# Performance work log

Hardware: AMD Instinct MI355X
Metric: run time of the kernel (lower is better)

## Reference

```python
import jax, jax.numpy as jnp
import numpy as np

B, S, D = 4, 4096, 128

def setup_inputs() -> dict:
    key = jax.random.key(0)
    kq, kk, kv = jax.random.split(key, 3)
    q = jax.random.normal(kq, (B, S, D), dtype=jnp.float32)
    k = jax.random.normal(kk, (B, S, D), dtype=jnp.float32)
    v = jax.random.normal(kv, (B, S, D), dtype=jnp.float32)
    return {"q": q, "k": k, "v": v}

def reference(q, k, v):
    d_model = q.shape[-1]
    scale = 1.0 / jnp.sqrt(jnp.asarray(d_model, q.dtype))
    # [B, S, S] scores
    scores = jnp.einsum('bqd,bkd->bqk', q, k) * scale
    s = q.shape[1]
    causal = jnp.tril(jnp.ones((s, s), dtype=bool))
    neg_inf = jnp.asarray(-jnp.inf, scores.dtype)
    scores = jnp.where(causal[None, :, :], scores, neg_inf)
    attn = jax.nn.softmax(scores, axis=-1)
    return jnp.einsum('bqk,bkd->bqd', attn, v)
```

## Files before the change

kernel.cpp:

```cpp
#include <hip/hip_runtime.h>


#define B_   4
#define S_   4096
#define D_   128
#define NT_  64
#define QT_  32
#define JB   128
#define W_   1056
#define SLOTS_PB 160
#define BLOB_SHORTS 16384
#define MASKVAL (-1.0e30f)

typedef __attribute__((ext_vector_type(8))) short bf16x8;
typedef __attribute__((ext_vector_type(4))) float f32x4;
typedef __attribute__((ext_vector_type(16))) float f32x16;

__device__ __forceinline__ short f2bf(float x) {
    unsigned u = __builtin_bit_cast(unsigned, x);
    unsigned r = (u + 0x7fffu + ((u >> 16) & 1u)) >> 16;
    return (short)r;
}
__device__ __forceinline__ float ex2(float x) { return __builtin_amdgcn_exp2f(x); }
__device__ __forceinline__ unsigned pkbf(float lo, float hi) {
    return (unsigned)(unsigned short)f2bf(lo) | ((unsigned)(unsigned short)f2bf(hi) << 16);
}
__device__ __forceinline__ float bf2f(short s) {
    return __builtin_bit_cast(float, ((unsigned)(unsigned short)s) << 16);
}
__device__ __forceinline__ void gl_lds16(const short* g, short* l) {
    __builtin_amdgcn_global_load_lds(
        (const __attribute__((address_space(1))) unsigned int*)g,
        (__attribute__((address_space(3))) unsigned int*)l, 16, 0, 0);
}
__device__ __forceinline__ int chunk_of(int v) { return (4 * v + 3) / 33; }

__global__ __launch_bounds__(256) void prep(const float* __restrict__ Qg,
                                            const float* __restrict__ Kg,
                                            const float* __restrict__ Vg,
                                            short* __restrict__ Qbf,
                                            short* __restrict__ KV)
{
    __shared__ short vt[64][40];
    const int id  = blockIdx.x;
    const int tid = threadIdx.x;
    const float SC = 0.12751740f;

    if (id < 1024) {
        const int b = id & 3, tile = (id >> 2) & 63, q4 = id >> 8;
        const int n = q4 * 16 + (tid >> 4);
        const int G = tid & 15;
        const size_t rowoff = ((size_t)b * S_ + (size_t)tile * 64 + n) * D_ + G * 8;
        short* blob = KV + (size_t)(b * NT_ + tile) * BLOB_SHORTS;
        {
            float4 a = *reinterpret_cast<const float4*>(Qg + rowoff);
            float4 c = *reinterpret_cast<const float4*>(Qg + rowoff + 4);
            bf16x8 v;
            v[0] = f2bf(a.x * SC); v[1] = f2bf(a.y * SC); v[2] = f2bf(a.z * SC); v[3] = f2bf(a.w * SC);
            v[4] = f2bf(c.x * SC); v[5] = f2bf(c.y * SC); v[6] = f2bf(c.z * SC); v[7] = f2bf(c.w * SC);
            *reinterpret_cast<bf16x8*>(Qbf + rowoff) = v;
        }
        {
            float4 a = *reinterpret_cast<const float4*>(Kg + rowoff);
            float4 c = *reinterpret_cast<const float4*>(Kg + rowoff + 4);
            bf16x8 v;
            v[0] = f2bf(a.x); v[1] = f2bf(a.y); v[2] = f2bf(a.z); v[3] = f2bf(a.w);
            v[4] = f2bf(c.x); v[5] = f2bf(c.y); v[6] = f2bf(c.z); v[7] = f2bf(c.w);
            const int p = (G & 8) | ((G & 7) ^ (n & 7));
            *reinterpret_cast<bf16x8*>(blob + n * 128 + p * 8) = v;
        }
    } else {
        const int u = id - 1024;
        const int b = u & 3, tile = (u >> 2) & 63, dq = u >> 8;
        short* blob = KV + (size_t)(b * NT_ + tile) * BLOB_SHORTS;
        {
            const int n = tid >> 2, c8 = tid & 3;
            const size_t off = ((size_t)b * S_ + (size_t)tile * 64 + n) * D_ + dq * 32 + c8 * 8;
            float4 a = *reinterpret_cast<const float4*>(Vg + off);
            float4 c = *reinterpret_cast<const float4*>(Vg + off + 4);
            bf16x8 v;
            v[0] = f2bf(a.x); v[1] = f2bf(a.y); v[2] = f2bf(a.z); v[3] = f2bf(a.w);
            v[4] = f2bf(c.x); v[5] = f2bf(c.y); v[6] = f2bf(c.z); v[7] = f2bf(c.w);
            *reinterpret_cast<bf16x8*>(&vt[n][c8 * 8]) = v;
        }
        __syncthreads();
        {
            const int dl = tid >> 3, G = tid & 7;
            const int d  = dq * 32 + dl;
            bf16x8 g;
#pragma unroll
            for (int i = 0; i < 8; ++i) g[i] = vt[G * 8 + i][dl];
            const int p = G ^ (d & 7);
            *reinterpret_cast<bf16x8*>(blob + 8192 + d * 64 + p * 8) = g;
        }
    }
}

__global__ __launch_bounds__(256, 2) void fa_bal(const short* __restrict__ Qbf,
                                                 const short* __restrict__ KV,
                                                 short* __restrict__ Opb,
                                                 float* __restrict__ Ml)
{
    __shared__ short lkv[2][BLOB_SHORTS];

    const int tid  = threadIdx.x;
    const int wv   = tid >> 6;
    const int lane = tid & 63;
    const int col  = lane & 31;
    const int half = lane >> 5;
    const int c7   = col & 7;

    const int batch = blockIdx.x & 3;
    const int j     = blockIdx.x >> 2;
    const int v0    = (33 * j) >> 2;
    const int v1    = (33 * (j + 1)) >> 2;

    int t = (int)((sqrtf((float)(4 * v0 + 1)) - 1.0f) * 0.5f);
    while ((t + 1) * (t + 2) <= v0) ++t;
    while (t * (t + 1) > v0) --t;
    int ktl = v0 - t * (t + 1);

    int base = 0;
    for (int tt = 0; tt < t; ++tt) {
        int a = chunk_of(tt * (tt + 1));
        int b2 = chunk_of((tt + 1) * (tt + 2) - 1);
        base += b2 - a + 1;
    }
    int slot = batch * SLOTS_PB + base + (j - chunk_of(t * (t + 1)));

    const size_t tilebase = (size_t)batch * NT_ * BLOB_SHORTS;
#define STAGE(KT, BUF) do {                                                   \
        const short* g_ = KV + tilebase + (size_t)(KT) * BLOB_SHORTS + tid * 8;\
        short* l_ = (BUF) + tid * 8;                                          \
        _Pragma("unroll")                                                     \
        for (int c_ = 0; c_ < 8; ++c_)                                        \
            gl_lds16(g_ + c_ * 2048, l_ + c_ * 2048);                         \
    } while (0)
#define LOADQ(T) do {                                                         \
        const short* qp_ = Qbf + ((size_t)batch * S_ + (size_t)(T) * 128      \
                                  + wv * 32 + col) * D_ + half * 8;           \
        _Pragma("unroll")                                                     \
        for (int c_ = 0; c_ < 8; ++c_)                                        \
            qf[c_] = *reinterpret_cast<const bf16x8*>(qp_ + c_ * 16);         \
    } while (0)

    bf16x8 qf[8];
    LOADQ(t);

    f32x16 acc[4];
#pragma unroll
    for (int i = 0; i < 4; ++i)
#pragma unroll
        for (int r = 0; r < 16; ++r) acc[i][r] = 0.f;
    float mrun = MASKVAL, lrun = 0.f;

    STAGE(ktl, lkv[0]);

    for (int v = v0; v < v1; ++v) {
        const short* cur = lkv[(v - v0) & 1];
        short* nxt = lkv[(v - v0 + 1) & 1];

        int nt = t, nktl = ktl + 1;
        if (nktl == 2 * t + 2) { nt = t + 1; nktl = 0; }

        __syncthreads();
        if (v + 1 < v1) STAGE(nktl, nxt);

        const short* lk = cur;
        const short* lv = cur + 8192;

        f32x16 st[2];
#pragma unroll
        for (int i = 0; i < 2; ++i)
#pragma unroll
            for (int r = 0; r < 16; ++r) st[i][r] = 0.f;
#pragma unroll
        for (int c = 0; c < 8; ++c) {
            const int G = 2 * c + half;
            const int p = (G & 8) | ((G & 7) ^ c7);
#pragma unroll
            for (int kt32 = 0; kt32 < 2; ++kt32) {
                const int n = kt32 * 32 + col;
                bf16x8 kf = *reinterpret_cast<const bf16x8*>(lk + n * 128 + p * 8);
                st[kt32] = __builtin_amdgcn_mfma_f32_32x32x16_bf16(kf, qf[c], st[kt32], 0, 0, 0);
            }
        }

        if (ktl >= 2 * t) {
            const int kbase = (ktl - 2 * t) * 64;
            const int qloc  = wv * 32 + col;
#pragma unroll
            for (int kt32 = 0; kt32 < 2; ++kt32)
#pragma unroll
                for (int r = 0; r < 16; ++r) {
                    const int kl = kt32 * 32 + (r & 3) + 8 * (r >> 2) + 4 * half;
                    if (kbase + kl > qloc) st[kt32][r] = MASKVAL;
                }
        }

        float mx = MASKVAL;
#pragma unroll
        for (int i = 0; i < 2; ++i)
#pragma unroll
            for (int r = 0; r < 16; ++r) mx = fmaxf(mx, st[i][r]);
        mx = fmaxf(mx, __shfl_xor(mx, 32));
        const float mnew = fmaxf(mrun, mx);
        const float al   = ex2(mrun - mnew);
        mrun = mnew;
        float sum = 0.f;
#pragma unroll
        for (int i = 0; i < 2; ++i)
#pragma unroll
            for (int r = 0; r < 16; ++r) {
                float pv = ex2(st[i][r] - mnew);
                st[i][r] = pv;
                sum += pv;
            }
        sum += __shfl_xor(sum, 32);
        lrun = lrun * al + sum;
#pragma unroll
        for (int i = 0; i < 4; ++i)
#pragma unroll
            for (int r = 0; r < 16; ++r) acc[i][r] *= al;

#pragma unroll
        for (int kt32 = 0; kt32 < 2; ++kt32) {
            unsigned pw[4][2];
#pragma unroll
            for (int w = 0; w < 4; ++w) {
                pw[w][0] = pkbf(st[kt32][4 * w],     st[kt32][4 * w + 1]);
                pw[w][1] = pkbf(st[kt32][4 * w + 2], st[kt32][4 * w + 3]);
            }
#pragma unroll
            for (int s1 = 0; s1 < 2; ++s1) {
                unsigned snd0 = pw[2 * s1 + 1 - half][0];
                unsigned snd1 = pw[2 * s1 + 1 - half][1];
                unsigned rcv0 = __shfl_xor((int)snd0, 32);
                unsigned rcv1 = __shfl_xor((int)snd1, 32);
                unsigned own0 = pw[2 * s1 + half][0];
                unsigned own1 = pw[2 * s1 + half][1];
                int4 wi;
                wi.x = (int)(half ? rcv0 : own0);
                wi.y = (int)(half ? rcv1 : own1);
                wi.z = (int)(half ? own0 : rcv0);
                wi.w = (int)(half ? own1 : rcv1);
                bf16x8 pf = __builtin_bit_cast(bf16x8, wi);
                const int G = 2 * (kt32 * 2 + s1) + half;
                const int p = G ^ c7;
#pragma unroll
                for (int dt = 0; dt < 4; ++dt) {
                    const int d = dt * 32 + col;
                    bf16x8 vf = *reinterpret_cast<const bf16x8*>(lv + d * 64 + p * 8);
                    acc[dt] = __builtin_amdgcn_mfma_f32_32x32x16_bf16(vf, pf, acc[dt], 0, 0, 0);
                }
            }
        }

        if (nktl == 0 || v + 1 == v1) {
            short* ob = Opb + (size_t)slot * (128 * D_) + tid * 64;
#pragma unroll
            for (int dt = 0; dt < 4; ++dt)
#pragma unroll
                for (int g = 0; g < 4; ++g) {
                    int2 w;
                    w.x = (int)pkbf(acc[dt][4 * g],     acc[dt][4 * g + 1]);
                    w.y = (int)pkbf(acc[dt][4 * g + 2], acc[dt][4 * g + 3]);
                    *reinterpret_cast<int2*>(ob + (dt * 4 + g) * 4) = w;
                }
            if (half == 0) {
                float* mlb = Ml + (size_t)slot * (128 * 2) + (wv * 32 + col) * 2;
                mlb[0] = mrun;
                mlb[1] = lrun;
            }
            if (v + 1 < v1) {
                int a = chunk_of(t * (t + 1));
                int b2 = chunk_of((t + 1) * (t + 2) - 1);
                base += b2 - a + 1;
                slot = batch * SLOTS_PB + base + (j - chunk_of(nt * (nt + 1)));
                LOADQ(nt);
#pragma unroll
                for (int i = 0; i < 4; ++i)
#pragma unroll
                    for (int r = 0; r < 16; ++r) acc[i][r] = 0.f;
                mrun = MASKVAL; lrun = 0.f;
            }
        }
        t = nt; ktl = nktl;
    }
#undef STAGE
#undef LOADQ
}

__global__ __launch_bounds__(256) void fa_merge(const short* __restrict__ Opb,
                                                const float* __restrict__ Ml,
                                                float* __restrict__ Og)
{
    const int x   = blockIdx.x;
    const int btq = x >> 4;
    const int oct = x & 15;
    const int b   = btq >> 5;
    const int t   = btq & (QT_ - 1);
    const int q   = oct * 8 + (threadIdx.x >> 5);
    const int cg  = threadIdx.x & 31;

    const int jlo = chunk_of(t * (t + 1));
    const int jhi = chunk_of((t + 1) * (t + 2) - 1);
    const int cnt = jhi - jlo + 1;
    int base = 0;
    for (int tt = 0; tt < t; ++tt) {
        int a = chunk_of(tt * (tt + 1));
        int b2 = chunk_of((tt + 1) * (tt + 2) - 1);
        base += b2 - a + 1;
    }
    const int slot0 = b * SLOTS_PB + base;

    const int t_id  = (q >> 5) * 64 + (cg & 1) * 32 + (q & 31);
    const int inner = (cg >> 3) * 4 + ((cg >> 1) & 3);
    const int d0    = (cg >> 3) * 32 + ((cg >> 1) & 3) * 8 + (cg & 1) * 4;

    float mg = MASKVAL;
    for (int r = 0; r < cnt; ++r)
        mg = fmaxf(mg, Ml[(size_t)(slot0 + r) * (128 * 2) + q * 2]);
    float l = 0.f;
    f32x4 a = (f32x4){0.f, 0.f, 0.f, 0.f};
    for (int r = 0; r < cnt; ++r) {
        const size_t sl = (size_t)(slot0 + r);
        float mr = Ml[sl * (128 * 2) + q * 2];
        float lr = Ml[sl * (128 * 2) + q * 2 + 1];
        float w  = ex2(mr - mg);
        l += lr * w;
        short4 s = *reinterpret_cast<const short4*>(
            Opb + sl * (128 * D_) + t_id * 64 + inner * 4);
        a[0] += w * bf2f(s.x);
        a[1] += w * bf2f(s.y);
        a[2] += w * bf2f(s.z);
        a[3] += w * bf2f(s.w);
    }
    *reinterpret_cast<f32x4*>(Og + (size_t)btq * (128 * D_) + q * D_ + d0) = a * (1.0f / l);
}

__global__ __launch_bounds__(256, 2) void fa_direct(const short* __restrict__ Qbf,
                                                    const short* __restrict__ KV,
                                                    float* __restrict__ Og)
{
    __shared__ short lkv[2][BLOB_SHORTS];
    const int tid  = threadIdx.x;
    const int wv   = tid >> 6;
    const int lane = tid & 63;
    const int col  = lane & 31;
    const int half = lane >> 5;
    const int c7   = col & 7;
    const int batch = blockIdx.x & 3;
    const int t     = QT_ - 1 - (blockIdx.x >> 2);
    const int hi    = 2 * t + 2;

    bf16x8 qf[8];
    {
        const short* qp = Qbf + ((size_t)batch * S_ + (size_t)t * 128 + wv * 32 + col) * D_ + half * 8;
#pragma unroll
        for (int c = 0; c < 8; ++c) qf[c] = *reinterpret_cast<const bf16x8*>(qp + c * 16);
    }
    f32x16 acc[4];
#pragma unroll
    for (int i = 0; i < 4; ++i)
#pragma unroll
        for (int r = 0; r < 16; ++r) acc[i][r] = 0.f;
    float mrun = MASKVAL, lrun = 0.f;
    const size_t tilebase = (size_t)batch * NT_ * BLOB_SHORTS;
#define STAGE(KT, BUF) do {                                                   \
        const short* g_ = KV + tilebase + (size_t)(KT) * BLOB_SHORTS + tid * 8;\
        short* l_ = (BUF) + tid * 8;                                          \
        _Pragma("unroll")                                                     \
        for (int c_ = 0; c_ < 8; ++c_)                                        \
            gl_lds16(g_ + c_ * 2048, l_ + c_ * 2048);                         \
    } while (0)
    STAGE(0, lkv[0]);
    for (int kt = 0; kt < hi; ++kt) {
        const short* cur = lkv[kt & 1];
        short* nxt = lkv[(kt + 1) & 1];
        __syncthreads();
        if (kt + 1 < hi) STAGE(kt + 1, nxt);
        const short* lk = cur;
        const short* lv = cur + 8192;
        f32x16 st[2];
#pragma unroll
        for (int i = 0; i < 2; ++i)
#pragma unroll
            for (int r = 0; r < 16; ++r) st[i][r] = 0.f;
#pragma unroll
        for (int c = 0; c < 8; ++c) {
            const int G = 2 * c + half;
            const int p = (G & 8) | ((G & 7) ^ c7);
#pragma unroll
            for (int kt32 = 0; kt32 < 2; ++kt32) {
                const int n = kt32 * 32 + col;
                bf16x8 kf = *reinterpret_cast<const bf16x8*>(lk + n * 128 + p * 8);
                st[kt32] = __builtin_amdgcn_mfma_f32_32x32x16_bf16(kf, qf[c], st[kt32], 0, 0, 0);
            }
        }
        if (kt >= 2 * t) {
            const int kbase = (kt - 2 * t) * 64;
            const int qloc  = wv * 32 + col;
#pragma unroll
            for (int kt32 = 0; kt32 < 2; ++kt32)
#pragma unroll
                for (int r = 0; r < 16; ++r) {
                    const int kl = kt32 * 32 + (r & 3) + 8 * (r >> 2) + 4 * half;
                    if (kbase + kl > qloc) st[kt32][r] = MASKVAL;
                }
        }
        float mx = MASKVAL;
#pragma unroll
        for (int i = 0; i < 2; ++i)
#pragma unroll
            for (int r = 0; r < 16; ++r) mx = fmaxf(mx, st[i][r]);
        mx = fmaxf(mx, __shfl_xor(mx, 32));
        const float mnew = fmaxf(mrun, mx);
        const float al   = ex2(mrun - mnew);
        mrun = mnew;
        float sum = 0.f;
#pragma unroll
        for (int i = 0; i < 2; ++i)
#pragma unroll
            for (int r = 0; r < 16; ++r) {
                float pv = ex2(st[i][r] - mnew);
                st[i][r] = pv;
                sum += pv;
            }
        sum += __shfl_xor(sum, 32);
        lrun = lrun * al + sum;
#pragma unroll
        for (int i = 0; i < 4; ++i)
#pragma unroll
            for (int r = 0; r < 16; ++r) acc[i][r] *= al;
#pragma unroll
        for (int kt32 = 0; kt32 < 2; ++kt32) {
            unsigned pw[4][2];
#pragma unroll
            for (int w = 0; w < 4; ++w) {
                pw[w][0] = pkbf(st[kt32][4 * w],     st[kt32][4 * w + 1]);
                pw[w][1] = pkbf(st[kt32][4 * w + 2], st[kt32][4 * w + 3]);
            }
#pragma unroll
            for (int s1 = 0; s1 < 2; ++s1) {
                unsigned snd0 = pw[2 * s1 + 1 - half][0];
                unsigned snd1 = pw[2 * s1 + 1 - half][1];
                unsigned rcv0 = __shfl_xor((int)snd0, 32);
                unsigned rcv1 = __shfl_xor((int)snd1, 32);
                unsigned own0 = pw[2 * s1 + half][0];
                unsigned own1 = pw[2 * s1 + half][1];
                int4 wi;
                wi.x = (int)(half ? rcv0 : own0);
                wi.y = (int)(half ? rcv1 : own1);
                wi.z = (int)(half ? own0 : rcv0);
                wi.w = (int)(half ? own1 : rcv1);
                bf16x8 pf = __builtin_bit_cast(bf16x8, wi);
                const int G = 2 * (kt32 * 2 + s1) + half;
                const int p = G ^ c7;
#pragma unroll
                for (int dt = 0; dt < 4; ++dt) {
                    const int d = dt * 32 + col;
                    bf16x8 vf = *reinterpret_cast<const bf16x8*>(lv + d * 64 + p * 8);
                    acc[dt] = __builtin_amdgcn_mfma_f32_32x32x16_bf16(vf, pf, acc[dt], 0, 0, 0);
                }
            }
        }
    }
#undef STAGE
    const int qloc = wv * 32 + col;
    const float inv = 1.0f / lrun;
    float* og = Og + ((size_t)batch * S_ + (size_t)t * 128 + qloc) * D_;
#pragma unroll
    for (int dt = 0; dt < 4; ++dt)
#pragma unroll
        for (int g = 0; g < 4; ++g) {
            const int d0 = dt * 32 + 8 * g + 4 * half;
            f32x4 v4 = {acc[dt][4 * g] * inv, acc[dt][4 * g + 1] * inv,
                        acc[dt][4 * g + 2] * inv, acc[dt][4 * g + 3] * inv};
            *reinterpret_cast<f32x4*>(og + d0) = v4;
        }
}

extern "C" void kernel_launch(void* const* d_in, const int* in_sizes, int n_in,
                              void* d_out, int out_size, void* d_ws, size_t ws_size,
                              hipStream_t stream) {
    const float* q = (const float*)d_in[0];
    const float* k = (const float*)d_in[1];
    const float* v = (const float*)d_in[2];
    float* o = (float*)d_out;

    const size_t QBF_BYTES = (size_t)B_ * S_ * D_ * 2;
    const size_t KV_BYTES  = (size_t)B_ * NT_ * BLOB_SHORTS * 2;
    const size_t OP_BYTES  = (size_t)B_ * SLOTS_PB * 128 * D_ * 2;
    const size_t ML_BYTES  = (size_t)B_ * SLOTS_PB * 128 * 2 * 4;
    const size_t NEEDED    = QBF_BYTES + KV_BYTES + OP_BYTES + ML_BYTES;

    char* ws = (char*)d_ws;
    short* Qbf = (short*)ws;
    short* KV  = (short*)(ws + QBF_BYTES);

    prep<<<dim3(2048), 256, 0, stream>>>(q, k, v, Qbf, KV);

    if (ws_size >= NEEDED) {
        short* Opb = (short*)(ws + QBF_BYTES + KV_BYTES);
        float* Ml  = (float*)(ws + QBF_BYTES + KV_BYTES + OP_BYTES);
        fa_bal<<<dim3(B_ * JB), 256, 0, stream>>>(Qbf, KV, Opb, Ml);
        fa_merge<<<dim3(B_ * QT_ * 16), 256, 0, stream>>>(Opb, Ml, o);
    } else {
        fa_direct<<<dim3(B_ * QT_), 256, 0, stream>>>(Qbf, KV, o);
    }
}
```

Measured before the change: 124.6 us.

## Double query tile to 256 rows with 512-thread blocks in balanced attention

The query tile per block grows from 128 to 256 rows, using 8 waves in 512-thread blocks, so each staged K/V tile in LDS is reused by twice as many queries. The load-balanced work partition (chunk_of, the triangular tile indexing, slot layout) and the merge kernel are rewritten for 16 query tiles. The aim is to cut K/V staging traffic and synchronisation per unit of work. In exchange, blocks are larger and fewer, and the __launch_bounds__(512, 4) setting tightens the register budget, which could cause spills or lower occupancy.

```diff
diff --git a/kernel.cpp b/kernel.cpp
--- a/kernel.cpp
+++ b/kernel.cpp
@@ -5,9 +5,9 @@
 #define S_   4096
 #define D_   128
 #define NT_  64
-#define QT_  32
+#define QT2_ 16
 #define JB   128
-#define W_   1056
+#define W2_  544
 #define SLOTS_PB 160
 #define BLOB_SHORTS 16384
 #define MASKVAL (-1.0e30f)
@@ -33,7 +33,7 @@
         (const __attribute__((address_space(1))) unsigned int*)g,
         (__attribute__((address_space(3))) unsigned int*)l, 16, 0, 0);
 }
-__device__ __forceinline__ int chunk_of(int v) { return (4 * v + 3) / 33; }
+__device__ __forceinline__ int chunk_of(int v) { return (4 * v) / 17; }
 
 __global__ __launch_bounds__(256) void prep(const float* __restrict__ Qg,
                                             const float* __restrict__ Kg,
@@ -96,7 +96,7 @@
     }
 }
 
-__global__ __launch_bounds__(256, 2) void fa_bal(const short* __restrict__ Qbf,
+__global__ __launch_bounds__(512, 4) void fa_bal(const short* __restrict__ Qbf,
                                                  const short* __restrict__ KV,
                                                  short* __restrict__ Opb,
                                                  float* __restrict__ Ml)
@@ -112,32 +112,32 @@
 
     const int batch = blockIdx.x & 3;
     const int j     = blockIdx.x >> 2;
-    const int v0    = (33 * j) >> 2;
-    const int v1    = (33 * (j + 1)) >> 2;
-
-    int t = (int)((sqrtf((float)(4 * v0 + 1)) - 1.0f) * 0.5f);
-    while ((t + 1) * (t + 2) <= v0) ++t;
-    while (t * (t + 1) > v0) --t;
-    int ktl = v0 - t * (t + 1);
+    const int v0    = (17 * j + 3) >> 2;
+    const int v1    = (17 * (j + 1) + 3) >> 2;
+
+    int t = (int)((sqrtf((float)(2 * v0) + 1.0f) - 1.0f) * 0.5f);
+    while (2 * (t + 1) * (t + 2) <= v0) ++t;
+    while (t > 0 && 2 * t * (t + 1) > v0) --t;
+    int ktl = v0 - 2 * t * (t + 1);
 
     int base = 0;
     for (int tt = 0; tt < t; ++tt) {
-        int a = chunk_of(tt * (tt + 1));
-        int b2 = chunk_of((tt + 1) * (tt + 2) - 1);
+        int a  = chunk_of(2 * tt * (tt + 1));
+        int b2 = chunk_of(2 * (tt + 1) * (tt + 2) - 1);
         base += b2 - a + 1;
     }
-    int slot = batch * SLOTS_PB + base + (j - chunk_of(t * (t + 1)));
+    int slot = batch * SLOTS_PB + base + (j - chunk_of(2 * t * (t + 1)));
 
     const size_t tilebase = (size_t)batch * NT_ * BLOB_SHORTS;
 #define STAGE(KT, BUF) do {                                                   \
         const short* g_ = KV + tilebase + (size_t)(KT) * BLOB_SHORTS + tid * 8;\
         short* l_ = (BUF) + tid * 8;                                          \
         _Pragma("unroll")                                                     \
-        for (int c_ = 0; c_ < 8; ++c_)                                        \
-            gl_lds16(g_ + c_ * 2048, l_ + c_ * 2048);                         \
+        for (int c_ = 0; c_ < 4; ++c_)                                        \
+            gl_lds16(g_ + c_ * 4096, l_ + c_ * 4096);                         \
     } while (0)
 #define LOADQ(T) do {                                                         \
-        const short* qp_ = Qbf + ((size_t)batch * S_ + (size_t)(T) * 128      \
+        const short* qp_ = Qbf + ((size_t)batch * S_ + (size_t)(T) * 256      \
                                   + wv * 32 + col) * D_ + half * 8;           \
         _Pragma("unroll")                                                     \
         for (int c_ = 0; c_ < 8; ++c_)                                        \
@@ -161,7 +161,7 @@
         short* nxt = lkv[(v - v0 + 1) & 1];
 
         int nt = t, nktl = ktl + 1;
-        if (nktl == 2 * t + 2) { nt = t + 1; nktl = 0; }
+        if (nktl == 4 * t + 4) { nt = t + 1; nktl = 0; }
 
         __syncthreads();
         if (v + 1 < v1) STAGE(nktl, nxt);
@@ -186,8 +186,8 @@
             }
         }
 
-        if (ktl >= 2 * t) {
-            const int kbase = (ktl - 2 * t) * 64;
+        if (ktl >= 4 * t) {
+            const int kbase = (ktl - 4 * t) * 64;
             const int qloc  = wv * 32 + col;
 #pragma unroll
             for (int kt32 = 0; kt32 < 2; ++kt32)
@@ -257,7 +257,7 @@
         }
 
         if (nktl == 0 || v + 1 == v1) {
-            short* ob = Opb + (size_t)slot * (128 * D_) + tid * 64;
+            short* ob = Opb + (size_t)slot * (256 * D_) + tid * 64;
 #pragma unroll
             for (int dt = 0; dt < 4; ++dt)
 #pragma unroll
@@ -268,15 +268,15 @@
                     *reinterpret_cast<int2*>(ob + (dt * 4 + g) * 4) = w;
                 }
             if (half == 0) {
-                float* mlb = Ml + (size_t)slot * (128 * 2) + (wv * 32 + col) * 2;
+                float* mlb = Ml + (size_t)slot * (256 * 2) + (wv * 32 + col) * 2;
                 mlb[0] = mrun;
                 mlb[1] = lrun;
             }
             if (v + 1 < v1) {
-                int a = chunk_of(t * (t + 1));
-                int b2 = chunk_of((t + 1) * (t + 2) - 1);
+                int a  = chunk_of(2 * t * (t + 1));
+                int b2 = chunk_of(2 * (t + 1) * (t + 2) - 1);
                 base += b2 - a + 1;
-                slot = batch * SLOTS_PB + base + (j - chunk_of(nt * (nt + 1)));
+                slot = batch * SLOTS_PB + base + (j - chunk_of(2 * nt * (nt + 1)));
                 LOADQ(nt);
 #pragma unroll
                 for (int i = 0; i < 4; ++i)
@@ -296,20 +296,20 @@
                                                 float* __restrict__ Og)
 {
     const int x   = blockIdx.x;
-    const int btq = x >> 4;
-    const int oct = x & 15;
-    const int b   = btq >> 5;
-    const int t   = btq & (QT_ - 1);
+    const int btq = x >> 5;
+    const int oct = x & 31;
+    const int b   = btq >> 4;
+    const int t   = btq & (QT2_ - 1);
     const int q   = oct * 8 + (threadIdx.x >> 5);
     const int cg  = threadIdx.x & 31;
 
-    const int jlo = chunk_of(t * (t + 1));
-    const int jhi = chunk_of((t + 1) * (t + 2) - 1);
+    const int jlo = chunk_of(2 * t * (t + 1));
+    const int jhi = chunk_of(2 * (t + 1) * (t + 2) - 1);
     const int cnt = jhi - jlo + 1;
     int base = 0;
     for (int tt = 0; tt < t; ++tt) {
-        int a = chunk_of(tt * (tt + 1));
-        int b2 = chunk_of((tt + 1) * (tt + 2) - 1);
+        int a  = chunk_of(2 * tt * (tt + 1));
+        int b2 = chunk_of(2 * (tt + 1) * (tt + 2) - 1);
         base += b2 - a + 1;
     }
     const int slot0 = b * SLOTS_PB + base;
@@ -320,26 +320,26 @@
 
     float mg = MASKVAL;
     for (int r = 0; r < cnt; ++r)
-        mg = fmaxf(mg, Ml[(size_t)(slot0 + r) * (128 * 2) + q * 2]);
+        mg = fmaxf(mg, Ml[(size_t)(slot0 + r) * (256 * 2) + q * 2]);
     float l = 0.f;
     f32x4 a = (f32x4){0.f, 0.f, 0.f, 0.f};
     for (int r = 0; r < cnt; ++r) {
         const size_t sl = (size_t)(slot0 + r);
-        float mr = Ml[sl * (128 * 2) + q * 2];
-        float lr = Ml[sl * (128 * 2) + q * 2 + 1];
+        float mr = Ml[sl * (256 * 2) + q * 2];
+        float lr = Ml[sl * (256 * 2) + q * 2 + 1];
         float w  = ex2(mr - mg);
         l += lr * w;
         short4 s = *reinterpret_cast<const short4*>(
-            Opb + sl * (128 * D_) + t_id * 64 + inner * 4);
+            Opb + sl * (256 * D_) + t_id * 64 + inner * 4);
         a[0] += w * bf2f(s.x);
         a[1] += w * bf2f(s.y);
         a[2] += w * bf2f(s.z);
         a[3] += w * bf2f(s.w);
     }
-    *reinterpret_cast<f32x4*>(Og + (size_t)btq * (128 * D_) + q * D_ + d0) = a * (1.0f / l);
-}
-
-__global__ __launch_bounds__(256, 2) void fa_direct(const short* __restrict__ Qbf,
+    *reinterpret_cast<f32x4*>(Og + (size_t)btq * (256 * D_) + q * D_ + d0) = a * (1.0f / l);
+}
+
+__global__ __launch_bounds__(512, 4) void fa_direct(const short* __restrict__ Qbf,
                                                     const short* __restrict__ KV,
                                                     float* __restrict__ Og)
 {
@@ -351,12 +351,12 @@
     const int half = lane >> 5;
     const int c7   = col & 7;
     const int batch = blockIdx.x & 3;
-    const int t     = QT_ - 1 - (blockIdx.x >> 2);
-    const int hi    = 2 * t + 2;
+    const int t     = QT2_ - 1 - (blockIdx.x >> 2);
+    const int hi    = 4 * t + 4;
 
     bf16x8 qf[8];
     {
-        const short* qp = Qbf + ((size_t)batch * S_ + (size_t)t * 128 + wv * 32 + col) * D_ + half * 8;
+        const short* qp = Qbf + ((size_t)batch * S_ + (size_t)t * 256 + wv * 32 + col) * D_ + half * 8;
 #pragma unroll
         for (int c = 0; c < 8; ++c) qf[c] = *reinterpret_cast<const bf16x8*>(qp + c * 16);
     }
@@ -371,8 +371,8 @@
         const short* g_ = KV + tilebase + (size_t)(KT) * BLOB_SHORTS + tid * 8;\
         short* l_ = (BUF) + tid * 8;                                          \
         _Pragma("unroll")                                                     \
-        for (int c_ = 0; c_ < 8; ++c_)                                        \
-            gl_lds16(g_ + c_ * 2048, l_ + c_ * 2048);                         \
+        for (int c_ = 0; c_ < 4; ++c_)                                        \
+            gl_lds16(g_ + c_ * 4096, l_ + c_ * 4096);                         \
     } while (0)
     STAGE(0, lkv[0]);
     for (int kt = 0; kt < hi; ++kt) {
@@ -398,8 +398,8 @@
                 st[kt32] = __builtin_amdgcn_mfma_f32_32x32x16_bf16(kf, qf[c], st[kt32], 0, 0, 0);
             }
         }
-        if (kt >= 2 * t) {
-            const int kbase = (kt - 2 * t) * 64;
+        if (kt >= 4 * t) {
+            const int kbase = (kt - 4 * t) * 64;
             const int qloc  = wv * 32 + col;
 #pragma unroll
             for (int kt32 = 0; kt32 < 2; ++kt32)
@@ -469,7 +469,7 @@
 #undef STAGE
     const int qloc = wv * 32 + col;
     const float inv = 1.0f / lrun;
-    float* og = Og + ((size_t)batch * S_ + (size_t)t * 128 + qloc) * D_;
+    float* og = Og + ((size_t)batch * S_ + (size_t)t * 256 + qloc) * D_;
 #pragma unroll
     for (int dt = 0; dt < 4; ++dt)
 #pragma unroll
@@ -491,8 +491,8 @@
 
     const size_t QBF_BYTES = (size_t)B_ * S_ * D_ * 2;
     const size_t KV_BYTES  = (size_t)B_ * NT_ * BLOB_SHORTS * 2;
-    const size_t OP_BYTES  = (size_t)B_ * SLOTS_PB * 128 * D_ * 2;
-    const size_t ML_BYTES  = (size_t)B_ * SLOTS_PB * 128 * 2 * 4;
+    const size_t OP_BYTES  = (size_t)B_ * SLOTS_PB * 256 * D_ * 2;
+    const size_t ML_BYTES  = (size_t)B_ * SLOTS_PB * 256 * 2 * 4;
     const size_t NEEDED    = QBF_BYTES + KV_BYTES + OP_BYTES + ML_BYTES;
 
     char* ws = (char*)d_ws;
@@ -504,9 +504,9 @@
     if (ws_size >= NEEDED) {
         short* Opb = (short*)(ws + QBF_BYTES + KV_BYTES);
         float* Ml  = (float*)(ws + QBF_BYTES + KV_BYTES + OP_BYTES);
-        fa_bal<<<dim3(B_ * JB), 256, 0, stream>>>(Qbf, KV, Opb, Ml);
-        fa_merge<<<dim3(B_ * QT_ * 16), 256, 0, stream>>>(Opb, Ml, o);
+        fa_bal<<<dim3(B_ * JB), 512, 0, stream>>>(Qbf, KV, Opb, Ml);
+        fa_merge<<<dim3(B_ * QT2_ * 32), 256, 0, stream>>>(Opb, Ml, o);
     } else {
-        fa_direct<<<dim3(B_ * QT_), 256, 0, stream>>>(Qbf, KV, o);
-    }
-}
+        fa_direct<<<dim3(B_ * QT2_), 512, 0, stream>>>(Qbf, KV, o);
+    }
+}
```

Measured after the change: 155.0 us. +24.4%, slower.
